# Optimization experiments

Hardware: AMD Instinct MI355X
Metric: run time of the kernel (lower is better)

The kernel has to match this reference:

```python
import jax, jax.numpy as jnp
import numpy as np

N = 100000      # total nodes (batched graphs)
E = 1200000     # total edges
A = 256         # annotation size (hidden_size_orig)
H = 64          # gnn_h_size
T = 4           # num_edge_types
STEPS = 6       # num_timesteps
B = 64          # number of graphs in the batch
NUM_CLS = 2


def setup_inputs() -> dict:
    key = jax.random.key(0)
    ks = jax.random.split(key, 16)
    annotation = jax.random.normal(ks[0], (N, A), dtype=jnp.float32)
    src = jax.random.randint(ks[1], (E,), 0, N, dtype=jnp.int32)
    dst = jax.random.randint(ks[2], (E,), 0, N, dtype=jnp.int32)
    etypes = jax.random.randint(ks[3], (E,), 0, T, dtype=jnp.int32)
    graph_ids = jnp.sort(jax.random.randint(ks[4], (N,), 0, B, dtype=jnp.int32))

    def lin(k, fan_in, shape):
        return jax.random.normal(k, shape, dtype=jnp.float32) / np.sqrt(fan_in).astype(np.float32)

    params = {
        'reduce_W': lin(ks[5], A, (A, H)),
        'reduce_b': jnp.zeros((H,), jnp.float32),
        'edge_W': lin(ks[6], H, (T, H, H)),      # per-edge-type linear
        'edge_b': jnp.zeros((T, H), jnp.float32),
        'gru_Wi': lin(ks[7], H, (3 * H, H)),     # torch GRUCell layout: r,z,n
        'gru_bi': jnp.zeros((3 * H,), jnp.float32),
        'gru_Wh': lin(ks[8], H, (3 * H, H)),
        'gru_bh': jnp.zeros((3 * H,), jnp.float32),
        'gate_W': lin(ks[9], 2 * H, (2 * H, 1)),
        'gate_b': jnp.zeros((1,), jnp.float32),
        'out_W': lin(ks[10], 2 * H, (2 * H, NUM_CLS)),
        'out_b': jnp.zeros((NUM_CLS,), jnp.float32),
    }
    return dict(annotation=annotation, src=src, dst=dst, etypes=etypes,
                graph_ids=graph_ids, **params)


def reference(annotation, src, dst, etypes, graph_ids,
              reduce_W, reduce_b, edge_W, edge_b,
              gru_Wi, gru_bi, gru_Wh, gru_bh,
              gate_W, gate_b, out_W, out_b):
    # reduce_layer
    h0 = annotation @ reduce_W + reduce_b            # [N, H]

    def step(h, _):
        # per-edge-type linear on all nodes: [T, N, H]
        transformed = jnp.einsum('nh,thk->tnk', h, edge_W) + edge_b[:, None, :]
        msg = transformed[etypes, src]               # [E, H] gather per edge
        a = jax.ops.segment_sum(msg, dst, num_segments=N)  # scatter-add
        # GRUCell(a, h)
        gi = a @ gru_Wi.T + gru_bi
        gh = h @ gru_Wh.T + gru_bh
        i_r, i_z, i_n = jnp.split(gi, 3, axis=-1)
        h_r, h_z, h_n = jnp.split(gh, 3, axis=-1)
        r = jax.nn.sigmoid(i_r + h_r)
        z = jax.nn.sigmoid(i_z + h_z)
        n = jnp.tanh(i_n + r * h_n)
        h_new = (1.0 - z) * n + z * h
        return h_new, None

    h, _ = jax.lax.scan(step, h0, None, length=STEPS)

    feat = jnp.concatenate([h, h0], axis=-1)         # [N, 2H]

    # GlobalAttentionPooling: segment softmax over gate scores, weighted sum
    gate = feat @ gate_W + gate_b                    # [N, 1]
    gmax = jax.ops.segment_max(gate, graph_ids, num_segments=B)
    gmax = jnp.where(jnp.isfinite(gmax), gmax, 0.0)  # guard empty graphs
    e = jnp.exp(gate - gmax[graph_ids])
    denom = jax.ops.segment_sum(e, graph_ids, num_segments=B)
    alpha = e / denom[graph_ids]                     # [N, 1]
    readout = jax.ops.segment_sum(alpha * feat, graph_ids, num_segments=B)  # [B, 2H]

    logits = readout @ out_W + out_b                 # [B, 2]
    return logits
```

## Files before the change

### kernel.cpp

```cpp
#include <hip/hip_runtime.h>
#include <cstdint>
#include <cstddef>

#define N_NODES 100000
#define N_EDGES 1200000
#define ASIZE 256
#define HSIZE 64
#define NTYPES 4
#define NSTEPS 6
#define NGRAPH 64
#define PS 16

static __device__ __forceinline__ float sigmoidf_(float x) { return 1.0f / (1.0f + expf(-x)); }

__global__ void k_count(const int* __restrict__ dst, int* __restrict__ deg) {
    int e = blockIdx.x * 256 + threadIdx.x;
    if (e < N_EDGES) atomicAdd(&deg[dst[e]], 1);
}

__global__ void k_scan1(const int* __restrict__ deg, int* __restrict__ rs, int* __restrict__ part) {
    __shared__ int sh[256];
    int t = threadIdx.x;
    int base = blockIdx.x * 1024 + t * 4;
    int v0 = (base + 0 < N_NODES) ? deg[base + 0] : 0;
    int v1 = (base + 1 < N_NODES) ? deg[base + 1] : 0;
    int v2 = (base + 2 < N_NODES) ? deg[base + 2] : 0;
    int v3 = (base + 3 < N_NODES) ? deg[base + 3] : 0;
    int s = v0 + v1 + v2 + v3;
    sh[t] = s;
    __syncthreads();
    for (int off = 1; off < 256; off <<= 1) {
        int x = (t >= off) ? sh[t - off] : 0;
        __syncthreads();
        sh[t] += x;
        __syncthreads();
    }
    int excl = sh[t] - s;
    if (t == 255) part[blockIdx.x] = sh[255];
    if (base + 0 < N_NODES) rs[base + 0] = excl;
    if (base + 1 < N_NODES) rs[base + 1] = excl + v0;
    if (base + 2 < N_NODES) rs[base + 2] = excl + v0 + v1;
    if (base + 3 < N_NODES) rs[base + 3] = excl + v0 + v1 + v2;
}

__global__ void k_scan2(int* __restrict__ part, int* __restrict__ rs, int nb) {
    if (threadIdx.x == 0 && blockIdx.x == 0) {
        int run = 0;
        for (int i = 0; i < nb; ++i) { int v = part[i]; part[i] = run; run += v; }
        rs[N_NODES] = run;
    }
}

__global__ void k_scan3(int* __restrict__ rs, const int* __restrict__ part) {
    int i = blockIdx.x * 256 + threadIdx.x;
    if (i < N_NODES) rs[i] += part[i >> 10];
}

__global__ void k_fill(const int* __restrict__ src, const int* __restrict__ dst,
                       const int* __restrict__ ety, const int* __restrict__ rs,
                       int* __restrict__ cur, int* __restrict__ colidx) {
    int e = blockIdx.x * 256 + threadIdx.x;
    if (e < N_EDGES) {
        int d = dst[e];
        int pos = rs[d] + atomicAdd(&cur[d], 1);
        colidx[pos] = src[e] * 448 + 192 + ety[e] * 64;
    }
}

__global__ void k_prep2(const float* __restrict__ Wh, const float* __restrict__ Bh,
                        const float* __restrict__ eW, const float* __restrict__ eb,
                        const float* __restrict__ Wi, const float* __restrict__ Bi,
                        float* __restrict__ W448, float* __restrict__ bias448,
                        float* __restrict__ WiA, float* __restrict__ biA) {
    int idx = blockIdx.x * 256 + threadIdx.x;
    if (idx < 64 * 448) {
        int k = idx / 448, m = idx % 448;
        float v;
        if (m < 192) {
            int j = m / 3, g = m % 3;
            v = Wh[(g * 64 + j) * 64 + k];
        } else {
            v = eW[(size_t)(m - 192 >> 6) * 4096 + k * 64 + ((m - 192) & 63)];
        }
        W448[idx] = v;
    }
    if (idx < 64 * 192) {
        int k = idx / 192, m = idx % 192;
        int j = m / 3, g = m % 3;
        WiA[idx] = Wi[(g * 64 + j) * 64 + k];
    }
    if (idx < 448) {
        bias448[idx] = (idx < 192) ? Bh[(idx % 3) * 64 + idx / 3] : eb[idx - 192];
    }
    if (idx < 192) {
        biA[idx] = Bi[(idx % 3) * 64 + idx / 3];
    }
}

__global__ __launch_bounds__(256) void k_gemm_step(const float* __restrict__ X,
                                                   const float* __restrict__ W,
                                                   const float* __restrict__ bias,
                                                   float* __restrict__ Y) {
    __shared__ float sX[128 * 66];
    __shared__ float sW[64 * 64];
    int tid = threadIdx.x;
    int ntile = blockIdx.x * 128;
    int tc4 = (tid & 15) * 4;
    int tr = tid >> 4;
    int swr = tid >> 4;
    int swc = (tid & 15) * 4;

#pragma unroll
    for (int i = 0; i < 8; ++i) {
        int lin4 = (i * 256 + tid) * 4;
        int nl = lin4 >> 6, kk = lin4 & 63;
        int n = ntile + nl;
        float4 v = make_float4(0.f, 0.f, 0.f, 0.f);
        if (n < N_NODES) v = *(const float4*)(X + (size_t)n * 64 + kk);
        float* d = sX + nl * 66 + kk;
        d[0] = v.x; d[1] = v.y; d[2] = v.z; d[3] = v.w;
    }
    float4 wreg[4];
#pragma unroll
    for (int i = 0; i < 4; ++i)
        wreg[i] = *(const float4*)(W + (size_t)(i * 16 + swr) * 448 + swc);
#pragma unroll
    for (int i = 0; i < 4; ++i)
        *(float4*)(sW + (i * 16 + swr) * 64 + swc) = wreg[i];
    __syncthreads();

    const float* xr = sX + tr * 8 * 66;
    const float* wrp = sW + tc4;
    for (int m = 0; m < 7; ++m) {
        if (m < 6) {
#pragma unroll
            for (int i = 0; i < 4; ++i)
                wreg[i] = *(const float4*)(W + (size_t)(i * 16 + swr) * 448 + (m + 1) * 64 + swc);
        }
        float4 acc[8];
#pragma unroll
        for (int i = 0; i < 8; ++i) acc[i] = make_float4(0.f, 0.f, 0.f, 0.f);
        for (int kk = 0; kk < 64; kk += 2) {
            float4 wA = *(const float4*)(wrp + kk * 64);
            float4 wB = *(const float4*)(wrp + (kk + 1) * 64);
            float xA[8], xB[8];
#pragma unroll
            for (int i = 0; i < 8; ++i) { xA[i] = xr[i * 66 + kk]; xB[i] = xr[i * 66 + kk + 1]; }
#pragma unroll
            for (int i = 0; i < 8; ++i) {
                acc[i].x = fmaf(xA[i], wA.x, acc[i].x);
                acc[i].y = fmaf(xA[i], wA.y, acc[i].y);
                acc[i].z = fmaf(xA[i], wA.z, acc[i].z);
                acc[i].w = fmaf(xA[i], wA.w, acc[i].w);
            }
#pragma unroll
            for (int i = 0; i < 8; ++i) {
                acc[i].x = fmaf(xB[i], wB.x, acc[i].x);
                acc[i].y = fmaf(xB[i], wB.y, acc[i].y);
                acc[i].z = fmaf(xB[i], wB.z, acc[i].z);
                acc[i].w = fmaf(xB[i], wB.w, acc[i].w);
            }
        }
        float4 bv = *(const float4*)(bias + m * 64 + tc4);
        if (m < 6) {
            __syncthreads();
#pragma unroll
            for (int i = 0; i < 4; ++i)
                *(float4*)(sW + (i * 16 + swr) * 64 + swc) = wreg[i];
            __syncthreads();
        }
#pragma unroll
        for (int i = 0; i < 8; ++i) {
            int n = ntile + tr * 8 + i;
            if (n < N_NODES) {
                float4 y;
                y.x = acc[i].x + bv.x; y.y = acc[i].y + bv.y;
                y.z = acc[i].z + bv.z; y.w = acc[i].w + bv.w;
                *(float4*)(Y + (size_t)n * 448 + m * 64 + tc4) = y;
            }
        }
    }
}

__global__ __launch_bounds__(256) void k_gemm_red(const float* __restrict__ X,
                                                  const float* __restrict__ W,
                                                  const float* __restrict__ bias,
                                                  float* __restrict__ Y,
                                                  float* __restrict__ Y2) {
    __shared__ float sX[128 * 66];
    __shared__ float sW[64 * 64];
    int tid = threadIdx.x;
    int ntile = blockIdx.x * 128;
    int tc4 = (tid & 15) * 4;
    int tr = tid >> 4;
    int swr = tid >> 4;
    int swc = (tid & 15) * 4;

    float4 acc[8];
#pragma unroll
    for (int i = 0; i < 8; ++i) acc[i] = make_float4(0.f, 0.f, 0.f, 0.f);

    float4 xreg[8];
    float4 wreg[4];
#pragma unroll
    for (int i = 0; i < 8; ++i) {
        int lin4 = (i * 256 + tid) * 4;
        int nl = lin4 >> 6, kk = lin4 & 63;
        int n = ntile + nl;
        float4 v = make_float4(0.f, 0.f, 0.f, 0.f);
        if (n < N_NODES) v = *(const float4*)(X + (size_t)n * 256 + kk);
        xreg[i] = v;
    }
#pragma unroll
    for (int i = 0; i < 4; ++i)
        wreg[i] = *(const float4*)(W + (size_t)(i * 16 + swr) * 64 + swc);

    for (int kc = 0; kc < 4; ++kc) {
#pragma unroll
        for (int i = 0; i < 8; ++i) {
            int lin4 = (i * 256 + tid) * 4;
            int nl = lin4 >> 6, kk = lin4 & 63;
            float* d = sX + nl * 66 + kk;
            d[0] = xreg[i].x; d[1] = xreg[i].y; d[2] = xreg[i].z; d[3] = xreg[i].w;
        }
#pragma unroll
        for (int i = 0; i < 4; ++i)
            *(float4*)(sW + (i * 16 + swr) * 64 + swc) = wreg[i];
        __syncthreads();
        if (kc < 3) {
#pragma unroll
            for (int i = 0; i < 8; ++i) {
                int lin4 = (i * 256 + tid) * 4;
                int nl = lin4 >> 6, kk = lin4 & 63;
                int n = ntile + nl;
                float4 v = make_float4(0.f, 0.f, 0.f, 0.f);
                if (n < N_NODES) v = *(const float4*)(X + (size_t)n * 256 + (kc + 1) * 64 + kk);
                xreg[i] = v;
            }
#pragma unroll
            for (int i = 0; i < 4; ++i)
                wreg[i] = *(const float4*)(W + (size_t)((kc + 1) * 64 + i * 16 + swr) * 64 + swc);
        }
        const float* xr = sX + tr * 8 * 66;
        const float* wrp = sW + tc4;
        for (int kk = 0; kk < 64; kk += 2) {
            float4 wA = *(const float4*)(wrp + kk * 64);
            float4 wB = *(const float4*)(wrp + (kk + 1) * 64);
            float xA[8], xB[8];
#pragma unroll
            for (int i = 0; i < 8; ++i) { xA[i] = xr[i * 66 + kk]; xB[i] = xr[i * 66 + kk + 1]; }
#pragma unroll
            for (int i = 0; i < 8; ++i) {
                acc[i].x = fmaf(xA[i], wA.x, acc[i].x);
                acc[i].y = fmaf(xA[i], wA.y, acc[i].y);
                acc[i].z = fmaf(xA[i], wA.z, acc[i].z);
                acc[i].w = fmaf(xA[i], wA.w, acc[i].w);
            }
#pragma unroll
            for (int i = 0; i < 8; ++i) {
                acc[i].x = fmaf(xB[i], wB.x, acc[i].x);
                acc[i].y = fmaf(xB[i], wB.y, acc[i].y);
                acc[i].z = fmaf(xB[i], wB.z, acc[i].z);
                acc[i].w = fmaf(xB[i], wB.w, acc[i].w);
            }
        }
        if (kc < 3) __syncthreads();
    }
    float4 bv = *(const float4*)(bias + tc4);
#pragma unroll
    for (int i = 0; i < 8; ++i) {
        int n = ntile + tr * 8 + i;
        if (n < N_NODES) {
            float4 y;
            y.x = acc[i].x + bv.x; y.y = acc[i].y + bv.y;
            y.z = acc[i].z + bv.z; y.w = acc[i].w + bv.w;
            *(float4*)(Y + (size_t)n * 64 + tc4) = y;
            *(float4*)(Y2 + (size_t)n * 64 + tc4) = y;
        }
    }
}

__global__ void k_aggregate(const float* __restrict__ buf1, const int* __restrict__ rs,
                            const int* __restrict__ colidx, float* __restrict__ a) {
    int l = threadIdx.x & 63;
    int n = blockIdx.x * 4 + (threadIdx.x >> 6);
    int beg = rs[n], end = rs[n + 1];
    float a0 = 0.f, a1 = 0.f, a2 = 0.f, a3 = 0.f;
    int s = beg;
    for (; s + 3 < end; s += 4) {
        int c0 = colidx[s], c1 = colidx[s + 1], c2 = colidx[s + 2], c3 = colidx[s + 3];
        a0 += buf1[(size_t)c0 + l];
        a1 += buf1[(size_t)c1 + l];
        a2 += buf1[(size_t)c2 + l];
        a3 += buf1[(size_t)c3 + l];
    }
    for (; s < end; ++s) a0 += buf1[(size_t)colidx[s] + l];
    a[(size_t)n * 64 + l] = (a0 + a1) + (a2 + a3);
}

__global__ __launch_bounds__(256) void k_gruF(const float* __restrict__ A,
                                              const float* __restrict__ WiA,
                                              const float* __restrict__ biA,
                                              const float* __restrict__ buf1,
                                              float* __restrict__ H) {
    __shared__ float sX[64 * 34];
    __shared__ float sW[32 * 192];
    int tid = threadIdx.x;
    int ntile = blockIdx.x * 64;
    int tc = tid & 15;
    int tr = tid >> 4;
    float acc[4][12];
#pragma unroll
    for (int i = 0; i < 4; ++i)
#pragma unroll
        for (int c = 0; c < 12; ++c) acc[i][c] = 0.f;

    for (int kc = 0; kc < 2; ++kc) {
        if (kc) __syncthreads();
#pragma unroll
        for (int i = 0; i < 2; ++i) {
            int lin4 = (i * 256 + tid) * 4;
            int nl = lin4 >> 5, kk = lin4 & 31;
            int n = ntile + nl;
            float4 v = make_float4(0.f, 0.f, 0.f, 0.f);
            if (n < N_NODES) v = *(const float4*)(A + (size_t)n * 64 + kc * 32 + kk);
            float* d = sX + nl * 34 + kk;
            d[0] = v.x; d[1] = v.y; d[2] = v.z; d[3] = v.w;
        }
        {
            int kk = tid >> 3, c = (tid & 7) * 24;
            const float* srcp = WiA + (size_t)(kc * 32 + kk) * 192 + c;
            float* d = sW + kk * 192 + c;
#pragma unroll
            for (int u = 0; u < 6; ++u) *(float4*)(d + 4 * u) = *(const float4*)(srcp + 4 * u);
        }
        __syncthreads();
        const float* xr = sX + tr * 4 * 34;
        const float* wr = sW + tc * 12;
        for (int kk = 0; kk < 32; kk += 2) {
            float4 w0 = *(const float4*)(wr + kk * 192);
            float4 w1 = *(const float4*)(wr + kk * 192 + 4);
            float4 w2 = *(const float4*)(wr + kk * 192 + 8);
            float4 u0 = *(const float4*)(wr + (kk + 1) * 192);
            float4 u1 = *(const float4*)(wr + (kk + 1) * 192 + 4);
            float4 u2 = *(const float4*)(wr + (kk + 1) * 192 + 8);
            float xA[4], xB[4];
#pragma unroll
            for (int i = 0; i < 4; ++i) { xA[i] = xr[i * 34 + kk]; xB[i] = xr[i * 34 + kk + 1]; }
#pragma unroll
            for (int i = 0; i < 4; ++i) {
                acc[i][0]  = fmaf(xA[i], w0.x, acc[i][0]);
                acc[i][1]  = fmaf(xA[i], w0.y, acc[i][1]);
                acc[i][2]  = fmaf(xA[i], w0.z, acc[i][2]);
                acc[i][3]  = fmaf(xA[i], w0.w, acc[i][3]);
                acc[i][4]  = fmaf(xA[i], w1.x, acc[i][4]);
                acc[i][5]  = fmaf(xA[i], w1.y, acc[i][5]);
                acc[i][6]  = fmaf(xA[i], w1.z, acc[i][6]);
                acc[i][7]  = fmaf(xA[i], w1.w, acc[i][7]);
                acc[i][8]  = fmaf(xA[i], w2.x, acc[i][8]);
                acc[i][9]  = fmaf(xA[i], w2.y, acc[i][9]);
                acc[i][10] = fmaf(xA[i], w2.z, acc[i][10]);
                acc[i][11] = fmaf(xA[i], w2.w, acc[i][11]);
            }
#pragma unroll
            for (int i = 0; i < 4; ++i) {
                acc[i][0]  = fmaf(xB[i], u0.x, acc[i][0]);
                acc[i][1]  = fmaf(xB[i], u0.y, acc[i][1]);
                acc[i][2]  = fmaf(xB[i], u0.z, acc[i][2]);
                acc[i][3]  = fmaf(xB[i], u0.w, acc[i][3]);
                acc[i][4]  = fmaf(xB[i], u1.x, acc[i][4]);
                acc[i][5]  = fmaf(xB[i], u1.y, acc[i][5]);
                acc[i][6]  = fmaf(xB[i], u1.z, acc[i][6]);
                acc[i][7]  = fmaf(xB[i], u1.w, acc[i][7]);
                acc[i][8]  = fmaf(xB[i], u2.x, acc[i][8]);
                acc[i][9]  = fmaf(xB[i], u2.y, acc[i][9]);
                acc[i][10] = fmaf(xB[i], u2.z, acc[i][10]);
                acc[i][11] = fmaf(xB[i], u2.w, acc[i][11]);
            }
        }
    }
    float bb[12];
    {
        float4 b0 = *(const float4*)(biA + tc * 12);
        float4 b1 = *(const float4*)(biA + tc * 12 + 4);
        float4 b2 = *(const float4*)(biA + tc * 12 + 8);
        bb[0] = b0.x; bb[1] = b0.y; bb[2] = b0.z; bb[3] = b0.w;
        bb[4] = b1.x; bb[5] = b1.y; bb[6] = b1.z; bb[7] = b1.w;
        bb[8] = b2.x; bb[9] = b2.y; bb[10] = b2.z; bb[11] = b2.w;
    }
#pragma unroll
    for (int i = 0; i < 4; ++i) {
        int n = ntile + tr * 4 + i;
        if (n >= N_NODES) continue;
        const float* ghp = buf1 + (size_t)n * 448 + tc * 12;
        float gg[12];
        float4 g0 = *(const float4*)(ghp);
        float4 g1 = *(const float4*)(ghp + 4);
        float4 g2 = *(const float4*)(ghp + 8);
        gg[0] = g0.x; gg[1] = g0.y; gg[2] = g0.z; gg[3] = g0.w;
        gg[4] = g1.x; gg[5] = g1.y; gg[6] = g1.z; gg[7] = g1.w;
        gg[8] = g2.x; gg[9] = g2.y; gg[10] = g2.z; gg[11] = g2.w;
        float4 hv = *(const float4*)(H + (size_t)n * 64 + tc * 4);
        float res[4];
#pragma unroll
        for (int jj = 0; jj < 4; ++jj) {
            int c = jj * 3;
            float r = sigmoidf_(acc[i][c] + bb[c] + gg[c]);
            float z = sigmoidf_(acc[i][c + 1] + bb[c + 1] + gg[c + 1]);
            float nn = tanhf(acc[i][c + 2] + bb[c + 2] + r * gg[c + 2]);
            float hj = (jj == 0) ? hv.x : (jj == 1) ? hv.y : (jj == 2) ? hv.z : hv.w;
            res[jj] = (1.f - z) * nn + z * hj;
        }
        float4 o; o.x = res[0]; o.y = res[1]; o.z = res[2]; o.w = res[3];
        *(float4*)(H + (size_t)n * 64 + tc * 4) = o;
    }
}

__global__ void k_bounds(const int* __restrict__ gid, int* __restrict__ start) {
    int n = blockIdx.x * 256 + threadIdx.x;
    if (n < N_NODES) {
        int g = gid[n];
        if (n == 0) {
            for (int x = 0; x <= g; ++x) start[x] = 0;
        } else {
            int pg = gid[n - 1];
            for (int x = pg + 1; x <= g; ++x) start[x] = n;
        }
        if (n == N_NODES - 1) {
            for (int x = g + 1; x <= NGRAPH; ++x) start[x] = N_NODES;
        }
    }
}

__global__ void k_gate2(const float* __restrict__ H, const float* __restrict__ H0,
                        const float* __restrict__ gW, const float* __restrict__ gb,
                        float* __restrict__ gate) {
    int l = threadIdx.x & 63;
    int n = blockIdx.x * 4 + (threadIdx.x >> 6);
    float v = H[(size_t)n * 64 + l] * gW[l] + H0[(size_t)n * 64 + l] * gW[64 + l];
    for (int off = 32; off > 0; off >>= 1) v += __shfl_xor(v, off, 64);
    if (l == 0) gate[n] = v + gb[0];
}

__global__ __launch_bounds__(64) void k_poolA(const float* __restrict__ gate,
                                              const int* __restrict__ start,
                                              float* __restrict__ pmax) {
    int g = blockIdx.x, s = blockIdx.y;
    int beg = start[g], len = start[g + 1] - beg;
    int sb = beg + (int)((long long)len * s / PS);
    int se = beg + (int)((long long)len * (s + 1) / PS);
    float m = -INFINITY;
    for (int n = sb + threadIdx.x; n < se; n += 64) m = fmaxf(m, gate[n]);
    for (int off = 32; off > 0; off >>= 1) m = fmaxf(m, __shfl_xor(m, off, 64));
    if (threadIdx.x == 0) pmax[g * PS + s] = m;
}

__global__ void k_poolB(const float* __restrict__ pmax, float* __restrict__ gm) {
    int g = threadIdx.x;
    float m = -INFINITY;
    for (int s = 0; s < PS; ++s) m = fmaxf(m, pmax[g * PS + s]);
    if (!isfinite(m)) m = 0.0f;
    gm[g] = m;
}

__global__ __launch_bounds__(256) void k_poolC(const float* __restrict__ H,
                                               const float* __restrict__ H0,
                                               const float* __restrict__ gate,
                                               const int* __restrict__ start,
                                               const float* __restrict__ gm,
                                               float* __restrict__ pnum,
                                               float* __restrict__ pden) {
    int g = blockIdx.x, s = blockIdx.y;
    int beg = start[g], len = start[g + 1] - beg;
    int sb = beg + (int)((long long)len * s / PS);
    int se = beg + (int)((long long)len * (s + 1) / PS);
    int t = threadIdx.x;
    int lane = t & 63, wave = t >> 6;
    float m = gm[g];
    __shared__ float shh[4][64], sh0[4][64], ses[4];
    float ah = 0.f, ah0 = 0.f, es = 0.f;
    for (int n = sb + wave; n < se; n += 4) {
        float e = expf(gate[n] - m);
        es += e;
        ah  += e * H [(size_t)n * 64 + lane];
        ah0 += e * H0[(size_t)n * 64 + lane];
    }
    shh[wave][lane] = ah; sh0[wave][lane] = ah0;
    if (lane == 0) ses[wave] = es;
    __syncthreads();
    if (wave == 0) {
        float r  = shh[0][lane] + shh[1][lane] + shh[2][lane] + shh[3][lane];
        float r0 = sh0[0][lane] + sh0[1][lane] + sh0[2][lane] + sh0[3][lane];
        int base = (g * PS + s) * 128;
        pnum[base + lane]      = r;
        pnum[base + 64 + lane] = r0;
        if (lane == 0) pden[g * PS + s] = ses[0] + ses[1] + ses[2] + ses[3];
    }
}

__global__ __launch_bounds__(128) void k_poolD(const float* __restrict__ pnum,
                                               const float* __restrict__ pden,
                                               float* __restrict__ ro) {
    int g = blockIdx.x;
    int c = threadIdx.x;
    float den = 0.f;
    for (int s = 0; s < PS; ++s) den += pden[g * PS + s];
    float nu = 0.f;
    for (int s = 0; s < PS; ++s) nu += pnum[(g * PS + s) * 128 + c];
    ro[g * 128 + c] = (den > 0.f) ? nu / den : 0.f;
}

__global__ void k_logits(const float* __restrict__ ro, const float* __restrict__ oW,
                         const float* __restrict__ ob, float* __restrict__ out) {
    int t = threadIdx.x;
    int b = t >> 1;
    int c = t & 1;
    float acc = ob[c];
    for (int k = 0; k < 128; ++k) acc = fmaf(ro[b * 128 + k], oW[k * 2 + c], acc);
    out[b * 2 + c] = acc;
}

extern "C" void kernel_launch(void* const* d_in, const int* in_sizes, int n_in,
                              void* d_out, int out_size, void* d_ws, size_t ws_size,
                              hipStream_t stream) {
    (void)in_sizes; (void)n_in; (void)out_size; (void)ws_size;
    const float* ann = (const float*)d_in[0];
    const int* src   = (const int*)d_in[1];
    const int* dst   = (const int*)d_in[2];
    const int* ety   = (const int*)d_in[3];
    const int* gid   = (const int*)d_in[4];
    const float* rW  = (const float*)d_in[5];
    const float* rb  = (const float*)d_in[6];
    const float* eW  = (const float*)d_in[7];
    const float* eb  = (const float*)d_in[8];
    const float* Wi  = (const float*)d_in[9];
    const float* Bi  = (const float*)d_in[10];
    const float* Wh  = (const float*)d_in[11];
    const float* Bh  = (const float*)d_in[12];
    const float* gW  = (const float*)d_in[13];
    const float* gb  = (const float*)d_in[14];
    const float* oW  = (const float*)d_in[15];
    const float* ob  = (const float*)d_in[16];
    float* out = (float*)d_out;

    char* p = (char*)d_ws;
    auto take = [&](size_t nbytes) -> void* {
        void* r = (void*)p;
        p += (nbytes + 255) & ~((size_t)255);
        return r;
    };
    float* h0      = (float*)take((size_t)N_NODES * 64 * 4);
    float* h       = (float*)take((size_t)N_NODES * 64 * 4);
    float* abuf    = (float*)take((size_t)N_NODES * 64 * 4);
    float* buf1    = (float*)take((size_t)N_NODES * 448 * 4);
    float* W448    = (float*)take(64 * 448 * 4);
    float* bias448 = (float*)take(448 * 4);
    float* WiA     = (float*)take(64 * 192 * 4);
    float* biA     = (float*)take(192 * 4);
    int* deg       = (int*)take((size_t)N_NODES * 4);
    int* cur       = (int*)take((size_t)N_NODES * 4);
    int* rs        = (int*)take((size_t)(N_NODES + 1) * 4);
    int* part      = (int*)take(512);
    int* colidx    = (int*)take((size_t)N_EDGES * 4);
    float* gate    = (float*)take((size_t)N_NODES * 4);
    int* start     = (int*)take((size_t)(NGRAPH + 1) * 4);
    float* pmax    = (float*)take(NGRAPH * PS * 4);
    float* gm      = (float*)take(NGRAPH * 4);
    float* pnum    = (float*)take((size_t)NGRAPH * PS * 128 * 4);
    float* pden    = (float*)take(NGRAPH * PS * 4);
    float* ro      = (float*)take(NGRAPH * 128 * 4);

    hipMemsetAsync(deg, 0, (size_t)N_NODES * 4, stream);
    hipMemsetAsync(cur, 0, (size_t)N_NODES * 4, stream);
    k_count<<<(N_EDGES + 255) / 256, 256, 0, stream>>>(dst, deg);
    int nb = (N_NODES + 1023) / 1024;
    k_scan1<<<nb, 256, 0, stream>>>(deg, rs, part);
    k_scan2<<<1, 64, 0, stream>>>(part, rs, nb);
    k_scan3<<<(N_NODES + 255) / 256, 256, 0, stream>>>(rs, part);
    k_fill<<<(N_EDGES + 255) / 256, 256, 0, stream>>>(src, dst, ety, rs, cur, colidx);

    k_prep2<<<112, 256, 0, stream>>>(Wh, Bh, eW, eb, Wi, Bi, W448, bias448, WiA, biA);
    k_bounds<<<(N_NODES + 255) / 256, 256, 0, stream>>>(gid, start);

    int ntiles = (N_NODES + 127) / 128;

    k_gemm_red<<<ntiles, 256, 0, stream>>>(ann, rW, rb, h, h0);

    for (int s = 0; s < NSTEPS; ++s) {
        k_gemm_step<<<ntiles, 256, 0, stream>>>(h, W448, bias448, buf1);
        k_aggregate<<<N_NODES / 4, 256, 0, stream>>>(buf1, rs, colidx, abuf);
        k_gruF<<<(N_NODES + 63) / 64, 256, 0, stream>>>(abuf, WiA, biA, buf1, h);
    }

    k_gate2<<<N_NODES / 4, 256, 0, stream>>>(h, h0, gW, gb, gate);
    k_poolA<<<dim3(NGRAPH, PS), 64, 0, stream>>>(gate, start, pmax);
    k_poolB<<<1, 64, 0, stream>>>(pmax, gm);
    k_poolC<<<dim3(NGRAPH, PS), 256, 0, stream>>>(h, h0, gate, start, gm, pnum, pden);
    k_poolD<<<NGRAPH, 128, 0, stream>>>(pnum, pden, ro);
    k_logits<<<1, 128, 0, stream>>>(ro, oW, ob, out);
}
```

Measured before the change: 1.721 ms.

## Move hidden-state GRU projection into GRU kernel and vectorize edge aggregation

```diff
diff --git a/kernel.cpp b/kernel.cpp
--- a/kernel.cpp
+++ b/kernel.cpp
@@ -63,86 +63,76 @@
     if (e < N_EDGES) {
         int d = dst[e];
         int pos = rs[d] + atomicAdd(&cur[d], 1);
-        colidx[pos] = src[e] * 448 + 192 + ety[e] * 64;
+        colidx[pos] = src[e] * 256 + ety[e] * 64;
     }
 }
 
 __global__ void k_prep2(const float* __restrict__ Wh, const float* __restrict__ Bh,
                         const float* __restrict__ eW, const float* __restrict__ eb,
                         const float* __restrict__ Wi, const float* __restrict__ Bi,
-                        float* __restrict__ W448, float* __restrict__ bias448,
+                        float* __restrict__ W256, float* __restrict__ b256,
+                        float* __restrict__ Wh192, float* __restrict__ bh192,
                         float* __restrict__ WiA, float* __restrict__ biA) {
     int idx = blockIdx.x * 256 + threadIdx.x;
-    if (idx < 64 * 448) {
-        int k = idx / 448, m = idx % 448;
-        float v;
-        if (m < 192) {
-            int j = m / 3, g = m % 3;
-            v = Wh[(g * 64 + j) * 64 + k];
-        } else {
-            v = eW[(size_t)(m - 192 >> 6) * 4096 + k * 64 + ((m - 192) & 63)];
-        }
-        W448[idx] = v;
+    if (idx < 64 * 256) {
+        int k = idx / 256, c = idx % 256;
+        W256[idx] = eW[(size_t)(c >> 6) * 4096 + k * 64 + (c & 63)];
     }
     if (idx < 64 * 192) {
         int k = idx / 192, m = idx % 192;
         int j = m / 3, g = m % 3;
-        WiA[idx] = Wi[(g * 64 + j) * 64 + k];
-    }
-    if (idx < 448) {
-        bias448[idx] = (idx < 192) ? Bh[(idx % 3) * 64 + idx / 3] : eb[idx - 192];
-    }
+        WiA[idx]   = Wi[(g * 64 + j) * 64 + k];
+        Wh192[idx] = Wh[(g * 64 + j) * 64 + k];
+    }
+    if (idx < 256) b256[idx] = eb[idx];
     if (idx < 192) {
-        biA[idx] = Bi[(idx % 3) * 64 + idx / 3];
-    }
-}
-
-__global__ __launch_bounds__(256) void k_gemm_step(const float* __restrict__ X,
-                                                   const float* __restrict__ W,
-                                                   const float* __restrict__ bias,
-                                                   float* __restrict__ Y) {
+        biA[idx]   = Bi[(idx % 3) * 64 + idx / 3];
+        bh192[idx] = Bh[(idx % 3) * 64 + idx / 3];
+    }
+}
+
+__global__ __launch_bounds__(256) void k_gemm(const float* __restrict__ X, int ldx, int K,
+                                              const float* __restrict__ W, int ldw,
+                                              const float* __restrict__ bias,
+                                              float* __restrict__ Y, float* __restrict__ Y2,
+                                              int M) {
     __shared__ float sX[128 * 66];
     __shared__ float sW[64 * 64];
     int tid = threadIdx.x;
-    int ntile = blockIdx.x * 128;
+    int mtile = blockIdx.x * 64;
+    int ntile = blockIdx.y * 128;
     int tc4 = (tid & 15) * 4;
     int tr = tid >> 4;
-    int swr = tid >> 4;
-    int swc = (tid & 15) * 4;
-
-#pragma unroll
-    for (int i = 0; i < 8; ++i) {
-        int lin4 = (i * 256 + tid) * 4;
-        int nl = lin4 >> 6, kk = lin4 & 63;
-        int n = ntile + nl;
-        float4 v = make_float4(0.f, 0.f, 0.f, 0.f);
-        if (n < N_NODES) v = *(const float4*)(X + (size_t)n * 64 + kk);
-        float* d = sX + nl * 66 + kk;
-        d[0] = v.x; d[1] = v.y; d[2] = v.z; d[3] = v.w;
-    }
-    float4 wreg[4];
-#pragma unroll
-    for (int i = 0; i < 4; ++i)
-        wreg[i] = *(const float4*)(W + (size_t)(i * 16 + swr) * 448 + swc);
-#pragma unroll
-    for (int i = 0; i < 4; ++i)
-        *(float4*)(sW + (i * 16 + swr) * 64 + swc) = wreg[i];
-    __syncthreads();
-
-    const float* xr = sX + tr * 8 * 66;
-    const float* wrp = sW + tc4;
-    for (int m = 0; m < 7; ++m) {
-        if (m < 6) {
-#pragma unroll
-            for (int i = 0; i < 4; ++i)
-                wreg[i] = *(const float4*)(W + (size_t)(i * 16 + swr) * 448 + (m + 1) * 64 + swc);
-        }
-        float4 acc[8];
-#pragma unroll
-        for (int i = 0; i < 8; ++i) acc[i] = make_float4(0.f, 0.f, 0.f, 0.f);
+    float4 acc[8];
+#pragma unroll
+    for (int i = 0; i < 8; ++i) acc[i] = make_float4(0.f, 0.f, 0.f, 0.f);
+
+    int nkc = K >> 6;
+    for (int kc = 0; kc < nkc; ++kc) {
+        if (kc) __syncthreads();
+#pragma unroll
+        for (int i = 0; i < 8; ++i) {
+            int lin4 = (i * 256 + tid) * 4;
+            int nl = lin4 >> 6, kk = lin4 & 63;
+            int n = ntile + nl;
+            float4 v = make_float4(0.f, 0.f, 0.f, 0.f);
+            if (n < N_NODES) v = *(const float4*)(X + (size_t)n * ldx + kc * 64 + kk);
+            float* d = sX + nl * 66 + kk;
+            d[0] = v.x; d[1] = v.y; d[2] = v.z; d[3] = v.w;
+        }
+#pragma unroll
+        for (int i = 0; i < 4; ++i) {
+            int lin4 = (i * 256 + tid) * 4;
+            int kk = lin4 >> 6, c = lin4 & 63;
+            float4 v = *(const float4*)(W + (size_t)(kc * 64 + kk) * ldw + mtile + c);
+            *(float4*)(sW + kk * 64 + c) = v;
+        }
+        __syncthreads();
+        const float* xr = sX + tr * 8 * 66;
+        const float* wr = sW + tc4;
         for (int kk = 0; kk < 64; kk += 2) {
-            float4 wA = *(const float4*)(wrp + kk * 64);
-            float4 wB = *(const float4*)(wrp + (kk + 1) * 64);
+            float4 wA = *(const float4*)(wr + kk * 64);
+            float4 wB = *(const float4*)(wr + (kk + 1) * 64);
             float xA[8], xB[8];
 #pragma unroll
             for (int i = 0; i < 8; ++i) { xA[i] = xr[i * 66 + kk]; xB[i] = xr[i * 66 + kk + 1]; }
@@ -161,23 +151,17 @@
                 acc[i].w = fmaf(xB[i], wB.w, acc[i].w);
             }
         }
-        float4 bv = *(const float4*)(bias + m * 64 + tc4);
-        if (m < 6) {
-            __syncthreads();
-#pragma unroll
-            for (int i = 0; i < 4; ++i)
-                *(float4*)(sW + (i * 16 + swr) * 64 + swc) = wreg[i];
-            __syncthreads();
-        }
-#pragma unroll
-        for (int i = 0; i < 8; ++i) {
-            int n = ntile + tr * 8 + i;
-            if (n < N_NODES) {
-                float4 y;
-                y.x = acc[i].x + bv.x; y.y = acc[i].y + bv.y;
-                y.z = acc[i].z + bv.z; y.w = acc[i].w + bv.w;
-                *(float4*)(Y + (size_t)n * 448 + m * 64 + tc4) = y;
-            }
+    }
+    float4 bv = *(const float4*)(bias + mtile + tc4);
+#pragma unroll
+    for (int i = 0; i < 8; ++i) {
+        int n = ntile + tr * 8 + i;
+        if (n < N_NODES) {
+            float4 y;
+            y.x = acc[i].x + bv.x; y.y = acc[i].y + bv.y;
+            y.z = acc[i].z + bv.z; y.w = acc[i].w + bv.w;
+            *(float4*)(Y + (size_t)n * M + mtile + tc4) = y;
+            if (Y2) *(float4*)(Y2 + (size_t)n * M + mtile + tc4) = y;
         }
     }
 }
@@ -284,102 +268,140 @@
                             const int* __restrict__ colidx, float* __restrict__ a) {
     int l = threadIdx.x & 63;
     int n = blockIdx.x * 4 + (threadIdx.x >> 6);
+    int sub = l >> 4;
+    int kq = (l & 15) * 4;
     int beg = rs[n], end = rs[n + 1];
-    float a0 = 0.f, a1 = 0.f, a2 = 0.f, a3 = 0.f;
+    float4 acc = make_float4(0.f, 0.f, 0.f, 0.f);
     int s = beg;
+    for (; s + 15 < end; s += 16) {
+        int c0 = colidx[s + sub];
+        int c1 = colidx[s + 4 + sub];
+        int c2 = colidx[s + 8 + sub];
+        int c3 = colidx[s + 12 + sub];
+        float4 v0 = *(const float4*)(buf1 + (size_t)c0 + kq);
+        float4 v1 = *(const float4*)(buf1 + (size_t)c1 + kq);
+        float4 v2 = *(const float4*)(buf1 + (size_t)c2 + kq);
+        float4 v3 = *(const float4*)(buf1 + (size_t)c3 + kq);
+        acc.x += v0.x; acc.y += v0.y; acc.z += v0.z; acc.w += v0.w;
+        acc.x += v1.x; acc.y += v1.y; acc.z += v1.z; acc.w += v1.w;
+        acc.x += v2.x; acc.y += v2.y; acc.z += v2.z; acc.w += v2.w;
+        acc.x += v3.x; acc.y += v3.y; acc.z += v3.z; acc.w += v3.w;
+    }
     for (; s + 3 < end; s += 4) {
-        int c0 = colidx[s], c1 = colidx[s + 1], c2 = colidx[s + 2], c3 = colidx[s + 3];
-        a0 += buf1[(size_t)c0 + l];
-        a1 += buf1[(size_t)c1 + l];
-        a2 += buf1[(size_t)c2 + l];
-        a3 += buf1[(size_t)c3 + l];
-    }
-    for (; s < end; ++s) a0 += buf1[(size_t)colidx[s] + l];
-    a[(size_t)n * 64 + l] = (a0 + a1) + (a2 + a3);
-}
-
-__global__ __launch_bounds__(256) void k_gruF(const float* __restrict__ A,
-                                              const float* __restrict__ WiA,
-                                              const float* __restrict__ biA,
-                                              const float* __restrict__ buf1,
-                                              float* __restrict__ H) {
+        int c = colidx[s + sub];
+        float4 v = *(const float4*)(buf1 + (size_t)c + kq);
+        acc.x += v.x; acc.y += v.y; acc.z += v.z; acc.w += v.w;
+    }
+    for (; s < end; ++s) {
+        if (sub == 0) {
+            int c = colidx[s];
+            float4 v = *(const float4*)(buf1 + (size_t)c + kq);
+            acc.x += v.x; acc.y += v.y; acc.z += v.z; acc.w += v.w;
+        }
+    }
+    float4 t;
+    t.x = acc.x + __shfl_xor(acc.x, 16, 64);
+    t.y = acc.y + __shfl_xor(acc.y, 16, 64);
+    t.z = acc.z + __shfl_xor(acc.z, 16, 64);
+    t.w = acc.w + __shfl_xor(acc.w, 16, 64);
+    float4 r;
+    r.x = t.x + __shfl_xor(t.x, 32, 64);
+    r.y = t.y + __shfl_xor(t.y, 32, 64);
+    r.z = t.z + __shfl_xor(t.z, 32, 64);
+    r.w = t.w + __shfl_xor(t.w, 32, 64);
+    if (sub == 0) *(float4*)(a + (size_t)n * 64 + kq) = r;
+}
+
+__global__ __launch_bounds__(256) void k_gruF2(const float* __restrict__ A,
+                                               const float* __restrict__ WiA,
+                                               const float* __restrict__ biA,
+                                               const float* __restrict__ Wh192,
+                                               const float* __restrict__ bh192,
+                                               float* __restrict__ H) {
     __shared__ float sX[64 * 34];
     __shared__ float sW[32 * 192];
     int tid = threadIdx.x;
     int ntile = blockIdx.x * 64;
     int tc = tid & 15;
     int tr = tid >> 4;
-    float acc[4][12];
-#pragma unroll
-    for (int i = 0; i < 4; ++i)
-#pragma unroll
-        for (int c = 0; c < 12; ++c) acc[i][c] = 0.f;
-
-    for (int kc = 0; kc < 2; ++kc) {
-        if (kc) __syncthreads();
-#pragma unroll
-        for (int i = 0; i < 2; ++i) {
-            int lin4 = (i * 256 + tid) * 4;
-            int nl = lin4 >> 5, kk = lin4 & 31;
-            int n = ntile + nl;
-            float4 v = make_float4(0.f, 0.f, 0.f, 0.f);
-            if (n < N_NODES) v = *(const float4*)(A + (size_t)n * 64 + kc * 32 + kk);
-            float* d = sX + nl * 34 + kk;
-            d[0] = v.x; d[1] = v.y; d[2] = v.z; d[3] = v.w;
-        }
-        {
-            int kk = tid >> 3, c = (tid & 7) * 24;
-            const float* srcp = WiA + (size_t)(kc * 32 + kk) * 192 + c;
-            float* d = sW + kk * 192 + c;
-#pragma unroll
-            for (int u = 0; u < 6; ++u) *(float4*)(d + 4 * u) = *(const float4*)(srcp + 4 * u);
-        }
-        __syncthreads();
-        const float* xr = sX + tr * 4 * 34;
-        const float* wr = sW + tc * 12;
-        for (int kk = 0; kk < 32; kk += 2) {
-            float4 w0 = *(const float4*)(wr + kk * 192);
-            float4 w1 = *(const float4*)(wr + kk * 192 + 4);
-            float4 w2 = *(const float4*)(wr + kk * 192 + 8);
-            float4 u0 = *(const float4*)(wr + (kk + 1) * 192);
-            float4 u1 = *(const float4*)(wr + (kk + 1) * 192 + 4);
-            float4 u2 = *(const float4*)(wr + (kk + 1) * 192 + 8);
-            float xA[4], xB[4];
-#pragma unroll
-            for (int i = 0; i < 4; ++i) { xA[i] = xr[i * 34 + kk]; xB[i] = xr[i * 34 + kk + 1]; }
-#pragma unroll
-            for (int i = 0; i < 4; ++i) {
-                acc[i][0]  = fmaf(xA[i], w0.x, acc[i][0]);
-                acc[i][1]  = fmaf(xA[i], w0.y, acc[i][1]);
-                acc[i][2]  = fmaf(xA[i], w0.z, acc[i][2]);
-                acc[i][3]  = fmaf(xA[i], w0.w, acc[i][3]);
-                acc[i][4]  = fmaf(xA[i], w1.x, acc[i][4]);
-                acc[i][5]  = fmaf(xA[i], w1.y, acc[i][5]);
-                acc[i][6]  = fmaf(xA[i], w1.z, acc[i][6]);
-                acc[i][7]  = fmaf(xA[i], w1.w, acc[i][7]);
-                acc[i][8]  = fmaf(xA[i], w2.x, acc[i][8]);
-                acc[i][9]  = fmaf(xA[i], w2.y, acc[i][9]);
-                acc[i][10] = fmaf(xA[i], w2.z, acc[i][10]);
-                acc[i][11] = fmaf(xA[i], w2.w, acc[i][11]);
-            }
-#pragma unroll
-            for (int i = 0; i < 4; ++i) {
-                acc[i][0]  = fmaf(xB[i], u0.x, acc[i][0]);
-                acc[i][1]  = fmaf(xB[i], u0.y, acc[i][1]);
-                acc[i][2]  = fmaf(xB[i], u0.z, acc[i][2]);
-                acc[i][3]  = fmaf(xB[i], u0.w, acc[i][3]);
-                acc[i][4]  = fmaf(xB[i], u1.x, acc[i][4]);
-                acc[i][5]  = fmaf(xB[i], u1.y, acc[i][5]);
-                acc[i][6]  = fmaf(xB[i], u1.z, acc[i][6]);
-                acc[i][7]  = fmaf(xB[i], u1.w, acc[i][7]);
-                acc[i][8]  = fmaf(xB[i], u2.x, acc[i][8]);
-                acc[i][9]  = fmaf(xB[i], u2.y, acc[i][9]);
-                acc[i][10] = fmaf(xB[i], u2.z, acc[i][10]);
-                acc[i][11] = fmaf(xB[i], u2.w, acc[i][11]);
-            }
-        }
-    }
-    float bb[12];
+    float acc[2][4][12];
+#pragma unroll
+    for (int p = 0; p < 2; ++p)
+#pragma unroll
+        for (int i = 0; i < 4; ++i)
+#pragma unroll
+            for (int c = 0; c < 12; ++c) acc[p][i][c] = 0.f;
+
+#pragma unroll
+    for (int ph = 0; ph < 2; ++ph) {
+        const float* Xsrc = (ph == 0) ? A : H;
+        const float* Wsrc = (ph == 0) ? WiA : Wh192;
+        for (int kc = 0; kc < 2; ++kc) {
+            if (ph || kc) __syncthreads();
+#pragma unroll
+            for (int i = 0; i < 2; ++i) {
+                int lin4 = (i * 256 + tid) * 4;
+                int nl = lin4 >> 5, kk = lin4 & 31;
+                int n = ntile + nl;
+                float4 v = make_float4(0.f, 0.f, 0.f, 0.f);
+                if (n < N_NODES) v = *(const float4*)(Xsrc + (size_t)n * 64 + kc * 32 + kk);
+                float* d = sX + nl * 34 + kk;
+                d[0] = v.x; d[1] = v.y; d[2] = v.z; d[3] = v.w;
+            }
+            {
+                int kk = tid >> 3, c = (tid & 7) * 24;
+                const float* srcp = Wsrc + (size_t)(kc * 32 + kk) * 192 + c;
+                float* d = sW + kk * 192 + c;
+#pragma unroll
+                for (int u = 0; u < 6; ++u) *(float4*)(d + 4 * u) = *(const float4*)(srcp + 4 * u);
+            }
+            __syncthreads();
+            const float* xr = sX + tr * 4 * 34;
+            const float* wr = sW + tc * 12;
+            for (int kk = 0; kk < 32; kk += 2) {
+                float4 w0 = *(const float4*)(wr + kk * 192);
+                float4 w1 = *(const float4*)(wr + kk * 192 + 4);
+                float4 w2 = *(const float4*)(wr + kk * 192 + 8);
+                float4 u0 = *(const float4*)(wr + (kk + 1) * 192);
+                float4 u1 = *(const float4*)(wr + (kk + 1) * 192 + 4);
+                float4 u2 = *(const float4*)(wr + (kk + 1) * 192 + 8);
+                float xA[4], xB[4];
+#pragma unroll
+                for (int i = 0; i < 4; ++i) { xA[i] = xr[i * 34 + kk]; xB[i] = xr[i * 34 + kk + 1]; }
+#pragma unroll
+                for (int i = 0; i < 4; ++i) {
+                    acc[ph][i][0]  = fmaf(xA[i], w0.x, acc[ph][i][0]);
+                    acc[ph][i][1]  = fmaf(xA[i], w0.y, acc[ph][i][1]);
+                    acc[ph][i][2]  = fmaf(xA[i], w0.z, acc[ph][i][2]);
+                    acc[ph][i][3]  = fmaf(xA[i], w0.w, acc[ph][i][3]);
+                    acc[ph][i][4]  = fmaf(xA[i], w1.x, acc[ph][i][4]);
+                    acc[ph][i][5]  = fmaf(xA[i], w1.y, acc[ph][i][5]);
+                    acc[ph][i][6]  = fmaf(xA[i], w1.z, acc[ph][i][6]);
+                    acc[ph][i][7]  = fmaf(xA[i], w1.w, acc[ph][i][7]);
+                    acc[ph][i][8]  = fmaf(xA[i], w2.x, acc[ph][i][8]);
+                    acc[ph][i][9]  = fmaf(xA[i], w2.y, acc[ph][i][9]);
+                    acc[ph][i][10] = fmaf(xA[i], w2.z, acc[ph][i][10]);
+                    acc[ph][i][11] = fmaf(xA[i], w2.w, acc[ph][i][11]);
+                }
+#pragma unroll
+                for (int i = 0; i < 4; ++i) {
+                    acc[ph][i][0]  = fmaf(xB[i], u0.x, acc[ph][i][0]);
+                    acc[ph][i][1]  = fmaf(xB[i], u0.y, acc[ph][i][1]);
+                    acc[ph][i][2]  = fmaf(xB[i], u0.z, acc[ph][i][2]);
+                    acc[ph][i][3]  = fmaf(xB[i], u0.w, acc[ph][i][3]);
+                    acc[ph][i][4]  = fmaf(xB[i], u1.x, acc[ph][i][4]);
+                    acc[ph][i][5]  = fmaf(xB[i], u1.y, acc[ph][i][5]);
+                    acc[ph][i][6]  = fmaf(xB[i], u1.z, acc[ph][i][6]);
+                    acc[ph][i][7]  = fmaf(xB[i], u1.w, acc[ph][i][7]);
+                    acc[ph][i][8]  = fmaf(xB[i], u2.x, acc[ph][i][8]);
+                    acc[ph][i][9]  = fmaf(xB[i], u2.y, acc[ph][i][9]);
+                    acc[ph][i][10] = fmaf(xB[i], u2.z, acc[ph][i][10]);
+                    acc[ph][i][11] = fmaf(xB[i], u2.w, acc[ph][i][11]);
+                }
+            }
+        }
+    }
+    float bb[12], bh[12];
     {
         float4 b0 = *(const float4*)(biA + tc * 12);
         float4 b1 = *(const float4*)(biA + tc * 12 + 4);
@@ -387,27 +409,28 @@
         bb[0] = b0.x; bb[1] = b0.y; bb[2] = b0.z; bb[3] = b0.w;
         bb[4] = b1.x; bb[5] = b1.y; bb[6] = b1.z; bb[7] = b1.w;
         bb[8] = b2.x; bb[9] = b2.y; bb[10] = b2.z; bb[11] = b2.w;
+        float4 c0 = *(const float4*)(bh192 + tc * 12);
+        float4 c1 = *(const float4*)(bh192 + tc * 12 + 4);
+        float4 c2 = *(const float4*)(bh192 + tc * 12 + 8);
+        bh[0] = c0.x; bh[1] = c0.y; bh[2] = c0.z; bh[3] = c0.w;
+        bh[4] = c1.x; bh[5] = c1.y; bh[6] = c1.z; bh[7] = c1.w;
+        bh[8] = c2.x; bh[9] = c2.y; bh[10] = c2.z; bh[11] = c2.w;
     }
 #pragma unroll
     for (int i = 0; i < 4; ++i) {
         int n = ntile + tr * 4 + i;
         if (n >= N_NODES) continue;
-        const float* ghp = buf1 + (size_t)n * 448 + tc * 12;
         float gg[12];
-        float4 g0 = *(const float4*)(ghp);
-        float4 g1 = *(const float4*)(ghp + 4);
-        float4 g2 = *(const float4*)(ghp + 8);
-        gg[0] = g0.x; gg[1] = g0.y; gg[2] = g0.z; gg[3] = g0.w;
-        gg[4] = g1.x; gg[5] = g1.y; gg[6] = g1.z; gg[7] = g1.w;
-        gg[8] = g2.x; gg[9] = g2.y; gg[10] = g2.z; gg[11] = g2.w;
+#pragma unroll
+        for (int c = 0; c < 12; ++c) gg[c] = acc[1][i][c] + bh[c];
         float4 hv = *(const float4*)(H + (size_t)n * 64 + tc * 4);
         float res[4];
 #pragma unroll
         for (int jj = 0; jj < 4; ++jj) {
             int c = jj * 3;
-            float r = sigmoidf_(acc[i][c] + bb[c] + gg[c]);
-            float z = sigmoidf_(acc[i][c + 1] + bb[c + 1] + gg[c + 1]);
-            float nn = tanhf(acc[i][c + 2] + bb[c + 2] + r * gg[c + 2]);
+            float r = sigmoidf_(acc[0][i][c] + bb[c] + gg[c]);
+            float z = sigmoidf_(acc[0][i][c + 1] + bb[c + 1] + gg[c + 1]);
+            float nn = tanhf(acc[0][i][c + 2] + bb[c + 2] + r * gg[c + 2]);
             float hj = (jj == 0) ? hv.x : (jj == 1) ? hv.y : (jj == 2) ? hv.z : hv.w;
             res[jj] = (1.f - z) * nn + z * hj;
         }
@@ -552,9 +575,11 @@
     float* h0      = (float*)take((size_t)N_NODES * 64 * 4);
     float* h       = (float*)take((size_t)N_NODES * 64 * 4);
     float* abuf    = (float*)take((size_t)N_NODES * 64 * 4);
-    float* buf1    = (float*)take((size_t)N_NODES * 448 * 4);
-    float* W448    = (float*)take(64 * 448 * 4);
-    float* bias448 = (float*)take(448 * 4);
+    float* buf1    = (float*)take((size_t)N_NODES * 256 * 4);
+    float* W256    = (float*)take(64 * 256 * 4);
+    float* b256    = (float*)take(256 * 4);
+    float* Wh192   = (float*)take(64 * 192 * 4);
+    float* bh192   = (float*)take(192 * 4);
     float* WiA     = (float*)take(64 * 192 * 4);
     float* biA     = (float*)take(192 * 4);
     int* deg       = (int*)take((size_t)N_NODES * 4);
@@ -579,7 +604,7 @@
     k_scan3<<<(N_NODES + 255) / 256, 256, 0, stream>>>(rs, part);
     k_fill<<<(N_EDGES + 255) / 256, 256, 0, stream>>>(src, dst, ety, rs, cur, colidx);
 
-    k_prep2<<<112, 256, 0, stream>>>(Wh, Bh, eW, eb, Wi, Bi, W448, bias448, WiA, biA);
+    k_prep2<<<112, 256, 0, stream>>>(Wh, Bh, eW, eb, Wi, Bi, W256, b256, Wh192, bh192, WiA, biA);
     k_bounds<<<(N_NODES + 255) / 256, 256, 0, stream>>>(gid, start);
 
     int ntiles = (N_NODES + 127) / 128;
@@ -587,9 +612,10 @@
     k_gemm_red<<<ntiles, 256, 0, stream>>>(ann, rW, rb, h, h0);
 
     for (int s = 0; s < NSTEPS; ++s) {
-        k_gemm_step<<<ntiles, 256, 0, stream>>>(h, W448, bias448, buf1);
+        k_gemm<<<dim3(4, ntiles), 256, 0, stream>>>(h, 64, 64, W256, 256, b256,
+                                                    buf1, nullptr, 256);
         k_aggregate<<<N_NODES / 4, 256, 0, stream>>>(buf1, rs, colidx, abuf);
-        k_gruF<<<(N_NODES + 63) / 64, 256, 0, stream>>>(abuf, WiA, biA, buf1, h);
+        k_gruF2<<<(N_NODES + 63) / 64, 256, 0, stream>>>(abuf, WiA, biA, Wh192, bh192, h);
     }
 
     k_gate2<<<N_NODES / 4, 256, 0, stream>>>(h, h0, gW, gb, gate);
```

After: 1.567 ms. -9.0%, faster.
